# Performance work log

Measured on AMD Instinct MI355X. Metric: run time of the kernel, lower is better.

Reference implementation:

```python
import jax, jax.numpy as jnp
import numpy as np

B, SENSORY, STATE, MOTOR = 4096, 64, 128, 32
ODE_UNFOLDS = 6
EPS = 1e-8
ELAPSED_TIME = 1.0


def setup_inputs() -> dict:
    key = jax.random.key(0)
    ks = jax.random.split(key, 20)
    u = lambda k, shape, lo, hi: jax.random.uniform(k, shape, jnp.float32, lo, hi)
    sign = lambda k, shape: jnp.where(jax.random.bernoulli(k, 0.5, shape), 1.0, -1.0).astype(jnp.float32)
    mask = lambda k, shape: (jax.random.uniform(k, shape) < 0.75).astype(jnp.float32)
    return {
        "inputs": jax.random.normal(ks[0], (B, SENSORY), jnp.float32),
        "states": jax.random.normal(ks[1], (B, STATE), jnp.float32),
        "gleak": u(ks[2], (STATE,), 0.001, 1.0),
        "vleak": u(ks[3], (STATE,), -0.2, 0.2),
        "cm": u(ks[4], (STATE,), 0.4, 0.6),
        "w": u(ks[5], (STATE, STATE), 0.001, 1.0),
        "sigma": u(ks[6], (STATE, STATE), 3.0, 8.0),
        "mu": u(ks[7], (STATE, STATE), 0.3, 0.8),
        "erev": sign(ks[8], (STATE, STATE)),
        "sensory_w": u(ks[9], (SENSORY, STATE), 0.001, 1.0),
        "sensory_sigma": u(ks[10], (SENSORY, STATE), 3.0, 8.0),
        "sensory_mu": u(ks[11], (SENSORY, STATE), 0.3, 0.8),
        "sensory_erev": sign(ks[12], (SENSORY, STATE)),
        "sparsity_mask": mask(ks[13], (STATE, STATE)),
        "sensory_sparsity_mask": mask(ks[14], (SENSORY, STATE)),
        "input_w": jnp.ones((SENSORY,), jnp.float32),
        "input_b": jnp.zeros((SENSORY,), jnp.float32),
        "output_w": jnp.ones((MOTOR,), jnp.float32),
        "output_b": jnp.zeros((MOTOR,), jnp.float32),
    }


def _syn_sigmoid(v_pre, mu, sigma):
    # v_pre: [B, P] -> [B, P, 1]; mu/sigma: [P, S]
    return jax.nn.sigmoid(sigma * (v_pre[..., None] - mu))


def reference(inputs, states, gleak, vleak, cm, w, sigma, mu, erev,
              sensory_w, sensory_sigma, sensory_mu, sensory_erev,
              sparsity_mask, sensory_sparsity_mask,
              input_w, input_b, output_w, output_b):
    # input mapping (affine); make_positive_fn = Identity (explicit constraints)
    x = inputs * input_w + input_b

    # sensory contributions (computed once, shared across unfolds)
    sens_act = sensory_w * _syn_sigmoid(x, sensory_mu, sensory_sigma)  # [B, In, S]
    sens_act = sens_act * sensory_sparsity_mask
    w_num_sensory = jnp.sum(sens_act * sensory_erev, axis=1)  # [B, S]
    w_den_sensory = jnp.sum(sens_act, axis=1)                 # [B, S]

    cm_t = cm / (ELAPSED_TIME / ODE_UNFOLDS)  # [S]

    v_pre = states
    for _ in range(ODE_UNFOLDS):
        w_act = w * _syn_sigmoid(v_pre, mu, sigma)   # [B, S, S]
        w_act = w_act * sparsity_mask
        w_numerator = jnp.sum(w_act * erev, axis=1) + w_num_sensory
        w_denominator = jnp.sum(w_act, axis=1) + w_den_sensory
        numerator = cm_t * v_pre + gleak * vleak + w_numerator
        denominator = cm_t + gleak + w_denominator
        v_pre = numerator / (denominator + EPS)

    # output mapping: slice motor neurons, then affine
    output = v_pre[:, :MOTOR] * output_w + output_b
    return output, v_pre
```

## Files before the change

kernel.cpp:

```cpp
#include <hip/hip_runtime.h>

#define LOG2E 1.4426950408889634f

constexpr int Bsz = 4096, Ssz = 128, Isz = 64, MOTOR = 32;
constexpr int BT = 4, NT = 128, R = 4;

__global__ void ltc_prep(const float* __restrict__ w, const float* __restrict__ sigma,
                         const float* __restrict__ mu, const float* __restrict__ erev,
                         const float* __restrict__ smask,
                         const float* __restrict__ sw, const float* __restrict__ ssig,
                         const float* __restrict__ smu, const float* __restrict__ serev,
                         const float* __restrict__ ssmask,
                         float4* __restrict__ Tm, float4* __restrict__ Ts)
{
  int idx = blockIdx.x * blockDim.x + threadIdx.x;
  if (idx < 32 * Ssz) {
    int q = idx >> 7, s = idx & 127;
    float4 a, b, wv;
    #pragma unroll
    for (int jj = 0; jj < 4; ++jj) {
      int e = (q * 4 + jj) * Ssz + s;
      float sg = sigma[e];
      (&a.x)[jj] = -sg * LOG2E;
      (&b.x)[jj] = sg * mu[e] * LOG2E;
      (&wv.x)[jj] = w[e] * smask[e] * erev[e];
    }
    Tm[(q * 3 + 0) * Ssz + s] = a;
    Tm[(q * 3 + 1) * Ssz + s] = b;
    Tm[(q * 3 + 2) * Ssz + s] = wv;
  } else if (idx < 32 * Ssz + 16 * Ssz) {
    int k = idx - 32 * Ssz;
    int q = k >> 7, s = k & 127;
    float4 a, b, wv;
    #pragma unroll
    for (int jj = 0; jj < 4; ++jj) {
      int e = (q * 4 + jj) * Ssz + s;
      float sg = ssig[e];
      (&a.x)[jj] = -sg * LOG2E;
      (&b.x)[jj] = sg * smu[e] * LOG2E;
      (&wv.x)[jj] = sw[e] * ssmask[e] * serev[e];
    }
    Ts[(q * 3 + 0) * Ssz + s] = a;
    Ts[(q * 3 + 1) * Ssz + s] = b;
    Ts[(q * 3 + 2) * Ssz + s] = wv;
  }
}

__launch_bounds__(NT, 4)
__global__ void ltc_main(const float* __restrict__ inputs, const float* __restrict__ states,
                         const float* __restrict__ gleak, const float* __restrict__ vleak,
                         const float* __restrict__ cmv,
                         const float* __restrict__ iw, const float* __restrict__ ib,
                         const float* __restrict__ ow, const float* __restrict__ ob,
                         const float4* __restrict__ Tm, const float4* __restrict__ Ts,
                         float* __restrict__ out)
{
  __shared__ float vsh[2][BT][Ssz];
  __shared__ float xsh[BT][Isz];

  const int t = threadIdx.x;
  const int s = t;
  const int b0 = blockIdx.x * BT;

  for (int k = t; k < BT * Isz; k += NT) {
    int r = k >> 6, i = k & 63;
    xsh[r][i] = inputs[(b0 + r) * Isz + i] * iw[i] + ib[i];
  }
  for (int k = t; k < BT * Ssz; k += NT) {
    int r = k >> 7, ss = k & 127;
    vsh[0][r][ss] = states[(b0 + r) * Ssz + ss];
  }
  const float cmt = cmv[s] * 6.0f;
  const float gl = gleak[s];
  const float gv = gl * vleak[s];
  const float dbase = cmt + gl + 1e-8f;
  __syncthreads();

  float sn[R] = {0.f, 0.f, 0.f, 0.f}, sd[R] = {0.f, 0.f, 0.f, 0.f};
  {
    const float4* pb = Ts + 1 * Ssz + s;
    #pragma unroll 2
    for (int q = 0; q < 16; ++q) {
      float4 a4 = pb[-Ssz], b4 = pb[0], w4 = pb[Ssz];
      pb += 3 * Ssz;
      #pragma unroll
      for (int r = 0; r < R; ++r) {
        float4 xq = *(const float4*)&xsh[r][q * 4];
        #pragma unroll
        for (int jj = 0; jj < 4; ++jj) {
          float arg = fmaf((&a4.x)[jj], (&xq.x)[jj], (&b4.x)[jj]);
          float u = __builtin_amdgcn_exp2f(arg);
          float sig = __builtin_amdgcn_rcpf(1.0f + u);
          sn[r] = fmaf((&w4.x)[jj], sig, sn[r]);
          sd[r] = fmaf(fabsf((&w4.x)[jj]), sig, sd[r]);
        }
      }
    }
  }

  #pragma unroll 1
  for (int it = 0; it < 6; ++it) {
    const int cur = it & 1;
    const float* vcur = &vsh[cur][0][0];
    float num[R], den[R];
    #pragma unroll
    for (int r = 0; r < R; ++r) { num[r] = sn[r]; den[r] = sd[r]; }

    const float4* pb = Tm + 1 * Ssz + s;
    #pragma unroll 2
    for (int q = 0; q < 32; ++q) {
      float4 a4 = pb[-Ssz], b4 = pb[0], w4 = pb[Ssz];
      pb += 3 * Ssz;
      #pragma unroll
      for (int r = 0; r < R; ++r) {
        float4 vq = *(const float4*)&vcur[r * Ssz + q * 4];
        #pragma unroll
        for (int jj = 0; jj < 4; ++jj) {
          float arg = fmaf((&a4.x)[jj], (&vq.x)[jj], (&b4.x)[jj]);
          float u = __builtin_amdgcn_exp2f(arg);
          float sig = __builtin_amdgcn_rcpf(1.0f + u);
          num[r] = fmaf((&w4.x)[jj], sig, num[r]);
          den[r] = fmaf(fabsf((&w4.x)[jj]), sig, den[r]);
        }
      }
    }

    #pragma unroll
    for (int r = 0; r < R; ++r) {
      float vo = vcur[r * Ssz + s];
      vsh[cur ^ 1][r][s] =
          (fmaf(cmt, vo, gv) + num[r]) * __builtin_amdgcn_rcpf(dbase + den[r]);
    }
    __syncthreads();
  }

  for (int k = t; k < BT * Ssz; k += NT) {
    int r = k >> 7, ss = k & 127;
    out[Bsz * MOTOR + (b0 + r) * Ssz + ss] = vsh[0][r][ss];
  }
  { int r = t >> 5, m = t & 31;
    out[(b0 + r) * MOTOR + m] = fmaf(vsh[0][r][m], ow[m], ob[m]); }
}

extern "C" void kernel_launch(void* const* d_in, const int* in_sizes, int n_in,
                              void* d_out, int out_size, void* d_ws, size_t ws_size,
                              hipStream_t stream) {
  const float* inputs = (const float*)d_in[0];
  const float* states = (const float*)d_in[1];
  const float* gleak  = (const float*)d_in[2];
  const float* vleak  = (const float*)d_in[3];
  const float* cmv    = (const float*)d_in[4];
  const float* w      = (const float*)d_in[5];
  const float* sigma  = (const float*)d_in[6];
  const float* mu     = (const float*)d_in[7];
  const float* erev   = (const float*)d_in[8];
  const float* sw     = (const float*)d_in[9];
  const float* ssig   = (const float*)d_in[10];
  const float* smu    = (const float*)d_in[11];
  const float* serev  = (const float*)d_in[12];
  const float* smask  = (const float*)d_in[13];
  const float* ssmask = (const float*)d_in[14];
  const float* iw     = (const float*)d_in[15];
  const float* ib     = (const float*)d_in[16];
  const float* ow     = (const float*)d_in[17];
  const float* ob     = (const float*)d_in[18];

  char* ws = (char*)d_ws;
  float4* Tm = (float4*)ws;
  float4* Ts = (float4*)(ws + 196608);
  float* out = (float*)d_out;

  constexpr int prep_items = 32 * Ssz + 16 * Ssz;
  ltc_prep<<<(prep_items + 255) / 256, 256, 0, stream>>>(
      w, sigma, mu, erev, smask, sw, ssig, smu, serev, ssmask, Tm, Ts);
  ltc_main<<<Bsz / BT, NT, 0, stream>>>(
      inputs, states, gleak, vleak, cmv, iw, ib, ow, ob, Tm, Ts, out);
}
```

Before: 119.2 us.

## Use single-wavefront blocks with two neurons per thread and drop barriers

Shrinks each block to one 64-lane wavefront covering 2 batch rows. Each lane computes two state neurons (s and s+64), and the state is kept in registers as well as shared memory. Because the block is a single wave, the double-buffered shared state and the per-iteration __syncthreads are removed, along with the staging loops for the output. In exchange, each table load is reused across only 2 batch rows instead of 4, so parameter-table traffic per batch row doubles. Correctness now depends on the single-wave assumption for shared-memory ordering.

```diff
diff --git a/kernel.cpp b/kernel.cpp
--- a/kernel.cpp
+++ b/kernel.cpp
@@ -3,7 +3,7 @@
 #define LOG2E 1.4426950408889634f
 
 constexpr int Bsz = 4096, Ssz = 128, Isz = 64, MOTOR = 32;
-constexpr int BT = 4, NT = 128, R = 4;
+constexpr int BT = 2, NT = 64;
 
 __global__ void ltc_prep(const float* __restrict__ w, const float* __restrict__ sigma,
                          const float* __restrict__ mu, const float* __restrict__ erev,
@@ -46,7 +46,7 @@
   }
 }
 
-__launch_bounds__(NT, 4)
+__launch_bounds__(NT, 2)
 __global__ void ltc_main(const float* __restrict__ inputs, const float* __restrict__ states,
                          const float* __restrict__ gleak, const float* __restrict__ vleak,
                          const float* __restrict__ cmv,
@@ -55,44 +55,57 @@
                          const float4* __restrict__ Tm, const float4* __restrict__ Ts,
                          float* __restrict__ out)
 {
-  __shared__ float vsh[2][BT][Ssz];
+  __shared__ float vsh[BT][Ssz];
   __shared__ float xsh[BT][Isz];
 
   const int t = threadIdx.x;
-  const int s = t;
+  const int s0 = t, s1 = t + 64;
   const int b0 = blockIdx.x * BT;
 
+  #pragma unroll
   for (int k = t; k < BT * Isz; k += NT) {
     int r = k >> 6, i = k & 63;
     xsh[r][i] = inputs[(b0 + r) * Isz + i] * iw[i] + ib[i];
   }
-  for (int k = t; k < BT * Ssz; k += NT) {
-    int r = k >> 7, ss = k & 127;
-    vsh[0][r][ss] = states[(b0 + r) * Ssz + ss];
-  }
-  const float cmt = cmv[s] * 6.0f;
-  const float gl = gleak[s];
-  const float gv = gl * vleak[s];
-  const float dbase = cmt + gl + 1e-8f;
-  __syncthreads();
-
-  float sn[R] = {0.f, 0.f, 0.f, 0.f}, sd[R] = {0.f, 0.f, 0.f, 0.f};
+  float vr0[BT], vr1[BT];
+  #pragma unroll
+  for (int r = 0; r < BT; ++r) {
+    vr0[r] = states[(b0 + r) * Ssz + s0];
+    vr1[r] = states[(b0 + r) * Ssz + s1];
+    vsh[r][s0] = vr0[r];
+    vsh[r][s1] = vr1[r];
+  }
+  const float cmt0 = cmv[s0] * 6.0f, cmt1 = cmv[s1] * 6.0f;
+  const float gl0 = gleak[s0], gl1 = gleak[s1];
+  const float gv0 = gl0 * vleak[s0], gv1 = gl1 * vleak[s1];
+  const float db0 = cmt0 + gl0 + 1e-8f, db1 = cmt1 + gl1 + 1e-8f;
+
+  float sn0[BT] = {0.f, 0.f}, sd0[BT] = {0.f, 0.f};
+  float sn1[BT] = {0.f, 0.f}, sd1[BT] = {0.f, 0.f};
   {
-    const float4* pb = Ts + 1 * Ssz + s;
+    const float4* pb = Ts + 1 * Ssz + s0;
     #pragma unroll 2
     for (int q = 0; q < 16; ++q) {
-      float4 a4 = pb[-Ssz], b4 = pb[0], w4 = pb[Ssz];
+      float4 aA = pb[-Ssz], aB = pb[-Ssz + 64];
+      float4 bA = pb[0],    bB = pb[64];
+      float4 wA = pb[Ssz],  wB = pb[Ssz + 64];
       pb += 3 * Ssz;
       #pragma unroll
-      for (int r = 0; r < R; ++r) {
+      for (int r = 0; r < BT; ++r) {
         float4 xq = *(const float4*)&xsh[r][q * 4];
         #pragma unroll
         for (int jj = 0; jj < 4; ++jj) {
-          float arg = fmaf((&a4.x)[jj], (&xq.x)[jj], (&b4.x)[jj]);
-          float u = __builtin_amdgcn_exp2f(arg);
-          float sig = __builtin_amdgcn_rcpf(1.0f + u);
-          sn[r] = fmaf((&w4.x)[jj], sig, sn[r]);
-          sd[r] = fmaf(fabsf((&w4.x)[jj]), sig, sd[r]);
+          float x = (&xq.x)[jj];
+          { float arg = fmaf((&aA.x)[jj], x, (&bA.x)[jj]);
+            float u = __builtin_amdgcn_exp2f(arg);
+            float sig = __builtin_amdgcn_rcpf(1.0f + u);
+            sn0[r] = fmaf((&wA.x)[jj], sig, sn0[r]);
+            sd0[r] = fmaf(fabsf((&wA.x)[jj]), sig, sd0[r]); }
+          { float arg = fmaf((&aB.x)[jj], x, (&bB.x)[jj]);
+            float u = __builtin_amdgcn_exp2f(arg);
+            float sig = __builtin_amdgcn_rcpf(1.0f + u);
+            sn1[r] = fmaf((&wB.x)[jj], sig, sn1[r]);
+            sd1[r] = fmaf(fabsf((&wB.x)[jj]), sig, sd1[r]); }
         }
       }
     }
@@ -100,46 +113,60 @@
 
   #pragma unroll 1
   for (int it = 0; it < 6; ++it) {
-    const int cur = it & 1;
-    const float* vcur = &vsh[cur][0][0];
-    float num[R], den[R];
-    #pragma unroll
-    for (int r = 0; r < R; ++r) { num[r] = sn[r]; den[r] = sd[r]; }
-
-    const float4* pb = Tm + 1 * Ssz + s;
+    float n0[BT], d0[BT], n1[BT], d1[BT];
+    #pragma unroll
+    for (int r = 0; r < BT; ++r) {
+      n0[r] = sn0[r]; d0[r] = sd0[r];
+      n1[r] = sn1[r]; d1[r] = sd1[r];
+    }
+
+    const float4* pq = Tm + 1 * Ssz + s0;
     #pragma unroll 2
     for (int q = 0; q < 32; ++q) {
-      float4 a4 = pb[-Ssz], b4 = pb[0], w4 = pb[Ssz];
-      pb += 3 * Ssz;
+      float4 aA = pq[-Ssz], aB = pq[-Ssz + 64];
+      float4 bA = pq[0],    bB = pq[64];
+      float4 wA = pq[Ssz],  wB = pq[Ssz + 64];
+      pq += 3 * Ssz;
       #pragma unroll
-      for (int r = 0; r < R; ++r) {
-        float4 vq = *(const float4*)&vcur[r * Ssz + q * 4];
+      for (int r = 0; r < BT; ++r) {
+        float4 vq = *(const float4*)&vsh[r][q * 4];
         #pragma unroll
         for (int jj = 0; jj < 4; ++jj) {
-          float arg = fmaf((&a4.x)[jj], (&vq.x)[jj], (&b4.x)[jj]);
-          float u = __builtin_amdgcn_exp2f(arg);
-          float sig = __builtin_amdgcn_rcpf(1.0f + u);
-          num[r] = fmaf((&w4.x)[jj], sig, num[r]);
-          den[r] = fmaf(fabsf((&w4.x)[jj]), sig, den[r]);
+          float v = (&vq.x)[jj];
+          { float arg = fmaf((&aA.x)[jj], v, (&bA.x)[jj]);
+            float u = __builtin_amdgcn_exp2f(arg);
+            float sig = __builtin_amdgcn_rcpf(1.0f + u);
+            n0[r] = fmaf((&wA.x)[jj], sig, n0[r]);
+            d0[r] = fmaf(fabsf((&wA.x)[jj]), sig, d0[r]); }
+          { float arg = fmaf((&aB.x)[jj], v, (&bB.x)[jj]);
+            float u = __builtin_amdgcn_exp2f(arg);
+            float sig = __builtin_amdgcn_rcpf(1.0f + u);
+            n1[r] = fmaf((&wB.x)[jj], sig, n1[r]);
+            d1[r] = fmaf(fabsf((&wB.x)[jj]), sig, d1[r]); }
         }
       }
     }
 
     #pragma unroll
-    for (int r = 0; r < R; ++r) {
-      float vo = vcur[r * Ssz + s];
-      vsh[cur ^ 1][r][s] =
-          (fmaf(cmt, vo, gv) + num[r]) * __builtin_amdgcn_rcpf(dbase + den[r]);
-    }
-    __syncthreads();
-  }
-
-  for (int k = t; k < BT * Ssz; k += NT) {
-    int r = k >> 7, ss = k & 127;
-    out[Bsz * MOTOR + (b0 + r) * Ssz + ss] = vsh[0][r][ss];
-  }
-  { int r = t >> 5, m = t & 31;
-    out[(b0 + r) * MOTOR + m] = fmaf(vsh[0][r][m], ow[m], ob[m]); }
+    for (int r = 0; r < BT; ++r) {
+      float u0 = (fmaf(cmt0, vr0[r], gv0) + n0[r]) * __builtin_amdgcn_rcpf(db0 + d0[r]);
+      float u1 = (fmaf(cmt1, vr1[r], gv1) + n1[r]) * __builtin_amdgcn_rcpf(db1 + d1[r]);
+      vr0[r] = u0; vr1[r] = u1;
+      vsh[r][s0] = u0; vsh[r][s1] = u1;
+    }
+  }
+
+  #pragma unroll
+  for (int r = 0; r < BT; ++r) {
+    out[Bsz * MOTOR + (b0 + r) * Ssz + s0] = vr0[r];
+    out[Bsz * MOTOR + (b0 + r) * Ssz + s1] = vr1[r];
+  }
+  if (t < MOTOR) {
+    float owm = ow[t], obm = ob[t];
+    #pragma unroll
+    for (int r = 0; r < BT; ++r)
+      out[(b0 + r) * MOTOR + t] = fmaf(vr0[r], owm, obm);
+  }
 }
 
 extern "C" void kernel_launch(void* const* d_in, const int* in_sizes, int n_in,
```

Measured after the change: 113.9 us. 4.4% less time.
